# Kernel tuning notes

Hardware: AMD Instinct MI355X
Metric: run time of the kernel (lower is better)

The kernel has to match this reference:

```python
import jax, jax.numpy as jnp
import numpy as np

B, C, D, W, H = 4, 64, 16, 32, 32
K = 2048  # codebook size

def setup_inputs() -> dict:
    key = jax.random.key(0)
    ks = jax.random.split(key, 6)
    return {
        "x": jax.random.normal(ks[0], (B, C, D, W, H), dtype=jnp.float32),
        "codebook": jax.random.normal(ks[1], (K, C), dtype=jnp.float32),
        "w_in": jax.random.normal(ks[2], (C, C), dtype=jnp.float32) * (1.0 / np.sqrt(C)),
        "b_in": jax.random.normal(ks[3], (C,), dtype=jnp.float32) * 0.01,
        "w_out": jax.random.normal(ks[4], (C, C), dtype=jnp.float32) * (1.0 / np.sqrt(C)),
        "b_out": jax.random.normal(ks[5], (C,), dtype=jnp.float32) * 0.01,
    }

def _conv1x1(x, w, b):
    # 1x1x1 Conv3d == channel mixing: x [B,C,D,W,H], w [Cout,Cin]
    return jnp.einsum('oc,bcdwh->bodwh', w, x) + b[None, :, None, None, None]

def _quantize(x, codebook):
    b, c, d, w, h = x.shape
    xf = jnp.moveaxis(x, 1, -1).reshape(b * d * w * h, c)  # [N, C] tokens
    # squared euclidean distances (same argmin as torch.cdist)
    d2 = (jnp.sum(xf * xf, axis=-1, keepdims=True)
          - 2.0 * xf @ codebook.T
          + jnp.sum(codebook * codebook, axis=-1)[None, :])  # [N, K]
    idx = jnp.argmin(d2, axis=-1)  # [N]
    q = codebook[idx]              # [N, C] gather
    sg = jax.lax.stop_gradient
    commitment_loss = jnp.mean((sg(q) - xf) ** 2)
    codebook_loss = jnp.mean((q - sg(xf)) ** 2)
    q_ste = xf + sg(q - xf)  # straight-through
    z = jnp.moveaxis(q_ste.reshape(b, d, w, h, c), -1, 1)  # [B,C,D,W,H]
    return z, codebook_loss, commitment_loss

def reference(x, codebook, w_in, b_in, w_out, b_out):
    pre = _conv1x1(x, w_in, b_in)
    z, cb_loss, cm_loss = _quantize(pre, codebook)
    out = _conv1x1(z, w_out, b_out)
    return out, z, cb_loss, cm_loss
```

## Files before the change

kernel.cpp:

```cpp
#include <hip/hip_runtime.h>

#define CC 64
#define SS 16384
#define NN 65536
#define KK 2048
#define BM 64
#define BMA 128

typedef __attribute__((ext_vector_type(8))) short bf16x8_t;
typedef __attribute__((ext_vector_type(4))) float fx4_t;
#define MFMA16 __builtin_amdgcn_mfma_f32_16x16x32_bf16

__device__ __forceinline__ unsigned short f2bf(float f) {
  unsigned u = __builtin_bit_cast(unsigned, f);
  return (unsigned short)((u + 0x7fff + ((u >> 16) & 1)) >> 16);
}
__device__ __forceinline__ float bf2f(unsigned short h) {
  unsigned u = (unsigned)h << 16;
  return __builtin_bit_cast(float, u);
}
__device__ __forceinline__ void glds16(const void* g, void* l) {
  __builtin_amdgcn_global_load_lds(
      (const __attribute__((address_space(1))) unsigned*)g,
      (__attribute__((address_space(3))) unsigned*)l, 16, 0, 0);
}

__global__ __launch_bounds__(256, 4) void vq_conv_in(
    const float* __restrict__ x, const float* __restrict__ w_in,
    const float* __restrict__ b_in, float* __restrict__ xf) {
  __shared__ float xs[CC][BM];
  __shared__ float wt[CC][CC];
  int t = threadIdx.x;
  int n0 = blockIdx.x * BM;
  int b = n0 >> 14, s0 = n0 & (SS - 1);
  {
    int o = t >> 2, c0 = (t & 3) * 16;
    const float4* wr = (const float4*)(w_in + o * CC + c0);
#pragma unroll
    for (int i = 0; i < 4; ++i) {
      float4 v = wr[i];
      int ci = c0 + 4 * i;
      wt[ci + 0][o] = v.x; wt[ci + 1][o] = v.y;
      wt[ci + 2][o] = v.z; wt[ci + 3][o] = v.w;
    }
  }
#pragma unroll
  for (int i = 0; i < 4; ++i) {
    int e4 = t + 256 * i;
    int ci = e4 >> 4, tok4 = (e4 & 15) * 4;
    *(float4*)&xs[ci][tok4] =
        *(const float4*)(x + (size_t)b * CC * SS + (size_t)ci * SS + s0 + tok4);
  }
  __syncthreads();
  int tx = t & 15, ty = t >> 4;
  double acc[4][4];
#pragma unroll
  for (int j = 0; j < 4; ++j) {
    double bj = (double)b_in[tx * 4 + j];
#pragma unroll
    for (int m = 0; m < 4; ++m) acc[m][j] = bj;
  }
#pragma unroll 8
  for (int ci = 0; ci < CC; ++ci) {
    float4 xq = *(const float4*)&xs[ci][ty * 4];
    float4 wq = *(const float4*)&wt[ci][tx * 4];
    double xm[4] = {xq.x, xq.y, xq.z, xq.w};
    double wm[4] = {wq.x, wq.y, wq.z, wq.w};
#pragma unroll
    for (int m = 0; m < 4; ++m)
#pragma unroll
      for (int j = 0; j < 4; ++j) acc[m][j] = fma(xm[m], wm[j], acc[m][j]);
  }
#pragma unroll
  for (int j = 0; j < 4; ++j) {
    float4 ov = make_float4((float)acc[0][j], (float)acc[1][j],
                            (float)acc[2][j], (float)acc[3][j]);
    *(float4*)(xf + (size_t)b * CC * SS + (size_t)(tx * 4 + j) * SS + s0 +
               ty * 4) = ov;
  }
}

__global__ __launch_bounds__(256) void vq_split(
    const float* __restrict__ cb, unsigned short* __restrict__ cbh,
    unsigned short* __restrict__ cbl, float* __restrict__ ch) {
  int k = blockIdx.x * 256 + threadIdx.x;
  const float4* r = (const float4*)(cb + (size_t)k * CC);
  unsigned* oh = (unsigned*)(cbh + (size_t)k * CC);
  unsigned* ol = (unsigned*)(cbl + (size_t)k * CC);
  float s = 0.f;
#pragma unroll
  for (int i = 0; i < 16; ++i) {
    float4 v = r[i];
    float vv[4] = {v.x, v.y, v.z, v.w};
    unsigned short h[4], l[4];
#pragma unroll
    for (int u = 0; u < 4; ++u) {
      s = fmaf(vv[u], vv[u], s);
      h[u] = f2bf(vv[u]);
      l[u] = f2bf(vv[u] - bf2f(h[u]));
    }
    oh[2 * i + 0] = (unsigned)h[0] | ((unsigned)h[1] << 16);
    oh[2 * i + 1] = (unsigned)h[2] | ((unsigned)h[3] << 16);
    ol[2 * i + 0] = (unsigned)l[0] | ((unsigned)l[1] << 16);
    ol[2 * i + 1] = (unsigned)l[2] | ((unsigned)l[3] << 16);
  }
  ch[k] = -0.5f * s;
}

__global__ __launch_bounds__(256, 4) void vq_mfma_argmin(
    const float* __restrict__ xf, const unsigned char* __restrict__ cbh,
    const unsigned char* __restrict__ cbl, const float* __restrict__ ch,
    int* __restrict__ cidx) {
  __shared__ __align__(16) unsigned char smem[36864];
  int t = threadIdx.x;
  int kh = blockIdx.x & 1;
  int n0 = (blockIdx.x >> 1) * BMA;
  int b = n0 >> 14, s0 = n0 & (SS - 1);
  int lane = t & 63, w = t >> 6;
  glds16((const unsigned char*)ch + kh * 4096 + w * 1024 + lane * 16,
         smem + 32768 + w * 1024);
  {
    int tok = t & 127;
    int half = t >> 7;
    const float* xb = xf + (size_t)b * CC * SS + s0 + tok;
#pragma unroll
    for (int i = 0; i < 4; ++i) {
      int c0 = half * 32 + i * 8;
      bf16x8_t h8, l8;
#pragma unroll
      for (int j = 0; j < 8; ++j) {
        float v = xb[(size_t)(c0 + j) * SS];
        unsigned short hs = f2bf(v);
        h8[j] = (short)hs;
        l8[j] = (short)f2bf(v - bf2f(hs));
      }
      int ad = tok * 128 + ((half * 64 + i * 16) ^ ((tok & 7) << 4));
      *(bf16x8_t*)(smem + ad) = h8;
      *(bf16x8_t*)(smem + 16384 + ad) = l8;
    }
  }
  __syncthreads();
  int col = lane & 15, quad = lane >> 4;
  bf16x8_t ah[2][2], al[2][2];
#pragma unroll
  for (int rt = 0; rt < 2; ++rt)
#pragma unroll
    for (int kk = 0; kk < 2; ++kk) {
      int tok = w * 32 + rt * 16 + col;
      int ad = tok * 128 + ((kk * 64 + quad * 16) ^ ((tok & 7) << 4));
      ah[rt][kk] = *(const bf16x8_t*)(smem + ad);
      al[rt][kk] = *(const bf16x8_t*)(smem + 16384 + ad);
    }
  __syncthreads();
  float best[2][4];
  int bi[2][4];
#pragma unroll
  for (int rt = 0; rt < 2; ++rt)
#pragma unroll
    for (int r = 0; r < 4; ++r) {
      best[rt][r] = -3.402823466e+38f;
      bi[rt][r] = 0;
    }
  int srcoff = (lane * 16) ^ (((lane >> 3) & 7) << 4);
  const unsigned char* ghh = cbh + (size_t)kh * 131072;
  const unsigned char* glh = cbl + (size_t)kh * 131072;
  glds16(ghh + w * 2048 + srcoff, smem + w * 2048);
  glds16(ghh + w * 2048 + 1024 + srcoff, smem + w * 2048 + 1024);
  glds16(glh + w * 2048 + srcoff, smem + 8192 + w * 2048);
  glds16(glh + w * 2048 + 1024 + srcoff, smem + 8192 + w * 2048 + 1024);
  __syncthreads();
  int swz = (col & 7) << 4;
  int cbo0 = col * 128 + ((quad * 16) ^ swz);
  int cbo1 = col * 128 + ((64 + quad * 16) ^ swz);
  int kcol = kh * 1024 + col;
  const int NT = 16;
  for (int kt = 0; kt < NT; ++kt) {
    unsigned char* bufc = smem + (kt & 1) * 16384;
    unsigned char* bufn = smem + ((kt + 1) & 1) * 16384;
    if (kt + 1 < NT) {
      size_t gof = (size_t)(kt + 1) * 8192 + w * 2048 + srcoff;
      glds16(ghh + gof, bufn + w * 2048);
      glds16(ghh + gof + 1024, bufn + w * 2048 + 1024);
      glds16(glh + gof, bufn + 8192 + w * 2048);
      glds16(glh + gof + 1024, bufn + 8192 + w * 2048 + 1024);
    }
    const unsigned char* cnb = smem + 32768 + kt * 256 + col * 4;
    int kbt = kcol + kt * 64;
#pragma unroll
    for (int sub = 0; sub < 4; ++sub) {
      bf16x8_t bh0 = *(const bf16x8_t*)(bufc + cbo0 + 2048 * sub);
      bf16x8_t bh1 = *(const bf16x8_t*)(bufc + cbo1 + 2048 * sub);
      bf16x8_t bl0 = *(const bf16x8_t*)(bufc + 8192 + cbo0 + 2048 * sub);
      bf16x8_t bl1 = *(const bf16x8_t*)(bufc + 8192 + cbo1 + 2048 * sub);
      float cn = *(const float*)(cnb + 64 * sub);
      int kbase = kbt + sub * 16;
#pragma unroll
      for (int rt = 0; rt < 2; ++rt) {
        fx4_t acc = {cn, cn, cn, cn};
        acc = MFMA16(al[rt][0], bh0, acc, 0, 0, 0);
        acc = MFMA16(al[rt][1], bh1, acc, 0, 0, 0);
        acc = MFMA16(ah[rt][0], bl0, acc, 0, 0, 0);
        acc = MFMA16(ah[rt][1], bl1, acc, 0, 0, 0);
        acc = MFMA16(ah[rt][0], bh0, acc, 0, 0, 0);
        acc = MFMA16(ah[rt][1], bh1, acc, 0, 0, 0);
#pragma unroll
        for (int r = 0; r < 4; ++r) {
          float v = acc[r];
          bool g = v > best[rt][r];
          best[rt][r] = g ? v : best[rt][r];
          bi[rt][r] = g ? kbase : bi[rt][r];
        }
      }
    }
    __syncthreads();
  }
  float secd[2][4];
  int si[2][4];
#pragma unroll
  for (int rt = 0; rt < 2; ++rt)
#pragma unroll
    for (int r = 0; r < 4; ++r) {
      secd[rt][r] = -3.402823466e+38f;
      si[rt][r] = 0x7fffffff;
    }
#pragma unroll
  for (int step = 1; step <= 8; step <<= 1) {
#pragma unroll
    for (int rt = 0; rt < 2; ++rt)
#pragma unroll
      for (int r = 0; r < 4; ++r) {
        float ob = __shfl_xor(best[rt][r], step, 64);
        int oi = __shfl_xor(bi[rt][r], step, 64);
        float os = __shfl_xor(secd[rt][r], step, 64);
        int oj = __shfl_xor(si[rt][r], step, 64);
        bool oW = (ob > best[rt][r]) || (ob == best[rt][r] && oi < bi[rt][r]);
        float nb = oW ? ob : best[rt][r];
        int ni = oW ? oi : bi[rt][r];
        float lb = oW ? best[rt][r] : ob;
        int li = oW ? bi[rt][r] : oi;
        float ws = oW ? os : secd[rt][r];
        int wi = oW ? oj : si[rt][r];
        bool sW = (ws > lb) || (ws == lb && wi < li);
        best[rt][r] = nb; bi[rt][r] = ni;
        secd[rt][r] = sW ? ws : lb; si[rt][r] = sW ? wi : li;
      }
  }
  if (col == 0) {
#pragma unroll
    for (int rt = 0; rt < 2; ++rt)
#pragma unroll
      for (int r = 0; r < 4; ++r) {
        int token = n0 + w * 32 + rt * 16 + quad * 4 + r;
        cidx[(size_t)(2 * kh + 0) * NN + token] = bi[rt][r];
        cidx[(size_t)(2 * kh + 1) * NN + token] = si[rt][r];
      }
  }
}

__global__ __launch_bounds__(256, 3) void vq_finish(
    const float* __restrict__ cb, const float* __restrict__ w_out,
    const float* __restrict__ b_out, const int* __restrict__ cidx,
    float* __restrict__ dout, float* __restrict__ loss_acc) {
  __shared__ float qs[CC][BM];
  __shared__ float xs[CC][BM];
  __shared__ float wt[CC][CC];
  __shared__ int ids[BM];
  int t = threadIdx.x;
  int n0 = blockIdx.x * BM;
  int b = n0 >> 14, s0 = n0 & (SS - 1);
  float* zreg = dout + (size_t)NN * CC;
  {
    int o = t >> 2, c0 = (t & 3) * 16;
    const float4* wr = (const float4*)(w_out + o * CC + c0);
#pragma unroll
    for (int i = 0; i < 4; ++i) {
      float4 v = wr[i];
      int ci = c0 + 4 * i;
      wt[ci + 0][o] = v.x; wt[ci + 1][o] = v.y;
      wt[ci + 2][o] = v.z; wt[ci + 3][o] = v.w;
    }
  }
#pragma unroll
  for (int i = 0; i < 4; ++i) {
    int e4 = t + 256 * i;
    int ci = e4 >> 4, tok4 = (e4 & 15) * 4;
    *(float4*)&xs[ci][tok4] = *(const float4*)(zreg + (size_t)b * CC * SS +
                                               (size_t)ci * SS + s0 + tok4);
  }
  __syncthreads();
  {
    int tok = t >> 2, cand = t & 3;
    int kj = cidx[(size_t)cand * NN + n0 + tok];
    const float* cp = cb + (size_t)kj * CC;
    double dj = 0.0;
#pragma unroll 8
    for (int c = 0; c < CC; ++c) {
      double df = (double)xs[c][tok] - (double)cp[c];
      dj = fma(df, df, dj);
    }
#pragma unroll
    for (int step = 1; step <= 2; step <<= 1) {
      double od = __shfl_xor(dj, step, 64);
      int ok = __shfl_xor(kj, step, 64);
      if (od < dj || (od == dj && ok < kj)) { dj = od; kj = ok; }
    }
    if (cand == 0) ids[tok] = kj;
  }
  __syncthreads();
  {
    int tok = t >> 2, c0 = (t & 3) * 16;
    const float4* qr = (const float4*)(cb + (size_t)ids[tok] * CC + c0);
#pragma unroll
    for (int i = 0; i < 4; ++i) {
      float4 v = qr[i];
      int ch = c0 + 4 * i;
      qs[ch + 0][tok] = v.x; qs[ch + 1][tok] = v.y;
      qs[ch + 2][tok] = v.z; qs[ch + 3][tok] = v.w;
    }
  }
  __syncthreads();
  float lsum = 0.f;
#pragma unroll
  for (int i = 0; i < 4; ++i) {
    int e4 = t + 256 * i;
    int ci = e4 >> 4, tok4 = (e4 & 15) * 4;
    float4 qv = *(const float4*)&qs[ci][tok4];
    float4 xv = *(const float4*)&xs[ci][tok4];
    float dx = qv.x - xv.x, dy = qv.y - xv.y;
    float dz = qv.z - xv.z, dw = qv.w - xv.w;
    lsum = fmaf(dx, dx, lsum); lsum = fmaf(dy, dy, lsum);
    lsum = fmaf(dz, dz, lsum); lsum = fmaf(dw, dw, lsum);
    *(float4*)(zreg + (size_t)b * CC * SS + (size_t)ci * SS + s0 + tok4) = qv;
  }
  int tx = t & 15, ty = t >> 4;
  float acc[4][4];
#pragma unroll
  for (int j = 0; j < 4; ++j) {
    float bj = b_out[tx * 4 + j];
#pragma unroll
    for (int m = 0; m < 4; ++m) acc[m][j] = bj;
  }
#pragma unroll 8
  for (int ci = 0; ci < CC; ++ci) {
    float4 xq = *(const float4*)&qs[ci][ty * 4];
    float4 wq = *(const float4*)&wt[ci][tx * 4];
    float xm[4] = {xq.x, xq.y, xq.z, xq.w};
    float wm[4] = {wq.x, wq.y, wq.z, wq.w};
#pragma unroll
    for (int m = 0; m < 4; ++m)
#pragma unroll
      for (int j = 0; j < 4; ++j) acc[m][j] = fmaf(xm[m], wm[j], acc[m][j]);
  }
#pragma unroll
  for (int j = 0; j < 4; ++j) {
    float4 ov = make_float4(acc[0][j], acc[1][j], acc[2][j], acc[3][j]);
    *(float4*)(dout + (size_t)b * CC * SS + (size_t)(tx * 4 + j) * SS + s0 +
               ty * 4) = ov;
  }
#pragma unroll
  for (int off = 32; off > 0; off >>= 1) lsum += __shfl_down(lsum, off, 64);
  __shared__ float wsum[4];
  if ((t & 63) == 0) wsum[t >> 6] = lsum;
  __syncthreads();
  if (t == 0) atomicAdd(loss_acc, wsum[0] + wsum[1] + wsum[2] + wsum[3]);
}

__global__ void vq_finalize(const float* __restrict__ loss_acc,
                            float* __restrict__ dout) {
  float l = loss_acc[0] * (1.0f / (float)((size_t)NN * CC));
  dout[(size_t)2 * NN * CC + 0] = l;
  dout[(size_t)2 * NN * CC + 1] = l;
}

extern "C" void kernel_launch(void* const* d_in, const int* in_sizes, int n_in,
                              void* d_out, int out_size, void* d_ws,
                              size_t ws_size, hipStream_t stream) {
  const float* x = (const float*)d_in[0];
  const float* cb = (const float*)d_in[1];
  const float* w_in = (const float*)d_in[2];
  const float* b_in = (const float*)d_in[3];
  const float* w_out = (const float*)d_in[4];
  const float* b_out = (const float*)d_in[5];
  float* out = (float*)d_out;
  float* zreg = out + (size_t)NN * CC;

  float* loss_acc = (float*)d_ws;
  float* ch = (float*)((char*)d_ws + 1024);
  unsigned short* cbh = (unsigned short*)((char*)d_ws + 16384);
  unsigned short* cbl = (unsigned short*)((char*)d_ws + 16384 + 262144);
  int* cidx = (int*)((char*)d_ws + 16384 + 2 * 262144);

  hipMemsetAsync(d_ws, 0, 4, stream);

  vq_conv_in<<<NN / BM, 256, 0, stream>>>(x, w_in, b_in, zreg);
  vq_split<<<KK / 256, 256, 0, stream>>>(cb, cbh, cbl, ch);
  vq_mfma_argmin<<<(NN / BMA) * 2, 256, 0, stream>>>(
      zreg, (const unsigned char*)cbh, (const unsigned char*)cbl, ch, cidx);
  vq_finish<<<NN / BM, 256, 0, stream>>>(cb, w_out, b_out, cidx, out,
                                         loss_acc);
  vq_finalize<<<1, 1, 0, stream>>>(loss_acc, out);
}
```

Measured before the change: 112.6 us.

## Triple-buffer codebook tiles with vmcnt waits and raise MFMA wave priority

```diff
diff --git a/kernel.cpp b/kernel.cpp
--- a/kernel.cpp
+++ b/kernel.cpp
@@ -111,14 +111,14 @@
     const float* __restrict__ xf, const unsigned char* __restrict__ cbh,
     const unsigned char* __restrict__ cbl, const float* __restrict__ ch,
     int* __restrict__ cidx) {
-  __shared__ __align__(16) unsigned char smem[36864];
+  __shared__ __align__(16) unsigned char smem[53248];
   int t = threadIdx.x;
   int kh = blockIdx.x & 1;
   int n0 = (blockIdx.x >> 1) * BMA;
   int b = n0 >> 14, s0 = n0 & (SS - 1);
   int lane = t & 63, w = t >> 6;
   glds16((const unsigned char*)ch + kh * 4096 + w * 1024 + lane * 16,
-         smem + 32768 + w * 1024);
+         smem + 49152 + w * 1024);
   {
     int tok = t & 127;
     int half = t >> 7;
@@ -164,27 +164,37 @@
   int srcoff = (lane * 16) ^ (((lane >> 3) & 7) << 4);
   const unsigned char* ghh = cbh + (size_t)kh * 131072;
   const unsigned char* glh = cbl + (size_t)kh * 131072;
-  glds16(ghh + w * 2048 + srcoff, smem + w * 2048);
-  glds16(ghh + w * 2048 + 1024 + srcoff, smem + w * 2048 + 1024);
-  glds16(glh + w * 2048 + srcoff, smem + 8192 + w * 2048);
-  glds16(glh + w * 2048 + 1024 + srcoff, smem + 8192 + w * 2048 + 1024);
-  __syncthreads();
+#pragma unroll
+  for (int p = 0; p < 2; ++p) {
+    size_t g = (size_t)p * 8192 + w * 2048 + srcoff;
+    unsigned boff = p * 16384;
+    glds16(ghh + g, smem + boff + w * 2048);
+    glds16(ghh + g + 1024, smem + boff + w * 2048 + 1024);
+    glds16(glh + g, smem + boff + 8192 + w * 2048);
+    glds16(glh + g + 1024, smem + boff + 8192 + w * 2048 + 1024);
+  }
   int swz = (col & 7) << 4;
   int cbo0 = col * 128 + ((quad * 16) ^ swz);
   int cbo1 = col * 128 + ((64 + quad * 16) ^ swz);
   int kcol = kh * 1024 + col;
   const int NT = 16;
+  int cur = 0;
   for (int kt = 0; kt < NT; ++kt) {
-    unsigned char* bufc = smem + (kt & 1) * 16384;
-    unsigned char* bufn = smem + ((kt + 1) & 1) * 16384;
-    if (kt + 1 < NT) {
-      size_t gof = (size_t)(kt + 1) * 8192 + w * 2048 + srcoff;
-      glds16(ghh + gof, bufn + w * 2048);
-      glds16(ghh + gof + 1024, bufn + w * 2048 + 1024);
-      glds16(glh + gof, bufn + 8192 + w * 2048);
-      glds16(glh + gof + 1024, bufn + 8192 + w * 2048 + 1024);
-    }
-    const unsigned char* cnb = smem + 32768 + kt * 256 + col * 4;
+    if (kt + 1 < NT)
+      asm volatile("s_waitcnt vmcnt(4)\n\ts_barrier" ::: "memory");
+    else
+      asm volatile("s_waitcnt vmcnt(0)\n\ts_barrier" ::: "memory");
+    if (kt + 2 < NT) {
+      int nb = cur + 2; if (nb >= 3) nb -= 3;
+      size_t g = (size_t)(kt + 2) * 8192 + w * 2048 + srcoff;
+      unsigned boff = nb * 16384;
+      glds16(ghh + g, smem + boff + w * 2048);
+      glds16(ghh + g + 1024, smem + boff + w * 2048 + 1024);
+      glds16(glh + g, smem + boff + 8192 + w * 2048);
+      glds16(glh + g + 1024, smem + boff + 8192 + w * 2048 + 1024);
+    }
+    unsigned char* bufc = smem + cur * 16384;
+    const unsigned char* cnb = smem + 49152 + kt * 256 + col * 4;
     int kbt = kcol + kt * 64;
 #pragma unroll
     for (int sub = 0; sub < 4; ++sub) {
@@ -197,12 +207,14 @@
 #pragma unroll
       for (int rt = 0; rt < 2; ++rt) {
         fx4_t acc = {cn, cn, cn, cn};
+        __builtin_amdgcn_s_setprio(1);
         acc = MFMA16(al[rt][0], bh0, acc, 0, 0, 0);
         acc = MFMA16(al[rt][1], bh1, acc, 0, 0, 0);
         acc = MFMA16(ah[rt][0], bl0, acc, 0, 0, 0);
         acc = MFMA16(ah[rt][1], bl1, acc, 0, 0, 0);
         acc = MFMA16(ah[rt][0], bh0, acc, 0, 0, 0);
         acc = MFMA16(ah[rt][1], bh1, acc, 0, 0, 0);
+        __builtin_amdgcn_s_setprio(0);
 #pragma unroll
         for (int r = 0; r < 4; ++r) {
           float v = acc[r];
@@ -212,7 +224,7 @@
         }
       }
     }
-    __syncthreads();
+    cur += 1; if (cur == 3) cur = 0;
   }
   float secd[2][4];
   int si[2][4];
```

After: 120.3 us. +6.8%, slower.

## Enlarge argmin token tile to 256 and split codebook into quarters

Applied to the files above, without the earlier changes.

```diff
diff --git a/kernel.cpp b/kernel.cpp
--- a/kernel.cpp
+++ b/kernel.cpp
@@ -5,7 +5,6 @@
 #define NN 65536
 #define KK 2048
 #define BM 64
-#define BMA 128
 
 typedef __attribute__((ext_vector_type(8))) short bf16x8_t;
 typedef __attribute__((ext_vector_type(4))) float fx4_t;
@@ -111,59 +110,66 @@
     const float* __restrict__ xf, const unsigned char* __restrict__ cbh,
     const unsigned char* __restrict__ cbl, const float* __restrict__ ch,
     int* __restrict__ cidx) {
-  __shared__ __align__(16) unsigned char smem[36864];
+  __shared__ __align__(16) unsigned char smem[34816];
   int t = threadIdx.x;
-  int kh = blockIdx.x & 1;
-  int n0 = (blockIdx.x >> 1) * BMA;
+  int q = blockIdx.x & 3;
+  int n0 = (blockIdx.x >> 2) * 256;
   int b = n0 >> 14, s0 = n0 & (SS - 1);
   int lane = t & 63, w = t >> 6;
-  glds16((const unsigned char*)ch + kh * 4096 + w * 1024 + lane * 16,
-         smem + 32768 + w * 1024);
-  {
-    int tok = t & 127;
-    int half = t >> 7;
-    const float* xb = xf + (size_t)b * CC * SS + s0 + tok;
-#pragma unroll
-    for (int i = 0; i < 4; ++i) {
-      int c0 = half * 32 + i * 8;
-      bf16x8_t h8, l8;
-#pragma unroll
-      for (int j = 0; j < 8; ++j) {
-        float v = xb[(size_t)(c0 + j) * SS];
-        unsigned short hs = f2bf(v);
-        h8[j] = (short)hs;
-        l8[j] = (short)f2bf(v - bf2f(hs));
+  int col = lane & 15, quad = lane >> 4;
+  if (w < 2)
+    glds16((const unsigned char*)ch + q * 2048 + w * 1024 + lane * 16,
+           smem + 32768 + w * 1024);
+  bf16x8_t ah[4][2], al[4][2];
+#pragma unroll
+  for (int rnd = 0; rnd < 2; ++rnd) {
+    {
+      int tokL = t & 127;
+      int half = t >> 7;
+      const float* xb = xf + (size_t)b * CC * SS + s0 + rnd * 128 + tokL;
+#pragma unroll
+      for (int i = 0; i < 4; ++i) {
+        int c0 = half * 32 + i * 8;
+        bf16x8_t h8, l8;
+#pragma unroll
+        for (int j = 0; j < 8; ++j) {
+          float v = xb[(size_t)(c0 + j) * SS];
+          unsigned short hs = f2bf(v);
+          h8[j] = (short)hs;
+          l8[j] = (short)f2bf(v - bf2f(hs));
+        }
+        int ad = tokL * 128 + ((half * 64 + i * 16) ^ ((tokL & 7) << 4));
+        *(bf16x8_t*)(smem + ad) = h8;
+        *(bf16x8_t*)(smem + 16384 + ad) = l8;
       }
-      int ad = tok * 128 + ((half * 64 + i * 16) ^ ((tok & 7) << 4));
-      *(bf16x8_t*)(smem + ad) = h8;
-      *(bf16x8_t*)(smem + 16384 + ad) = l8;
-    }
-  }
-  __syncthreads();
-  int col = lane & 15, quad = lane >> 4;
-  bf16x8_t ah[2][2], al[2][2];
-#pragma unroll
-  for (int rt = 0; rt < 2; ++rt)
-#pragma unroll
-    for (int kk = 0; kk < 2; ++kk) {
-      int tok = w * 32 + rt * 16 + col;
-      int ad = tok * 128 + ((kk * 64 + quad * 16) ^ ((tok & 7) << 4));
-      ah[rt][kk] = *(const bf16x8_t*)(smem + ad);
-      al[rt][kk] = *(const bf16x8_t*)(smem + 16384 + ad);
-    }
-  __syncthreads();
-  float best[2][4];
-  int bi[2][4];
-#pragma unroll
-  for (int rt = 0; rt < 2; ++rt)
+    }
+    __syncthreads();
+    if ((w >> 1) == rnd) {
+      int base = (w & 1) * 64;
+#pragma unroll
+      for (int rt = 0; rt < 4; ++rt)
+#pragma unroll
+        for (int kk = 0; kk < 2; ++kk) {
+          int tokL = base + rt * 16 + col;
+          int ad = tokL * 128 + ((kk * 64 + quad * 16) ^ ((tokL & 7) << 4));
+          ah[rt][kk] = *(const bf16x8_t*)(smem + ad);
+          al[rt][kk] = *(const bf16x8_t*)(smem + 16384 + ad);
+        }
+    }
+    __syncthreads();
+  }
+  float best[4][4];
+  int bi[4][4];
+#pragma unroll
+  for (int rt = 0; rt < 4; ++rt)
 #pragma unroll
     for (int r = 0; r < 4; ++r) {
       best[rt][r] = -3.402823466e+38f;
       bi[rt][r] = 0;
     }
   int srcoff = (lane * 16) ^ (((lane >> 3) & 7) << 4);
-  const unsigned char* ghh = cbh + (size_t)kh * 131072;
-  const unsigned char* glh = cbl + (size_t)kh * 131072;
+  const unsigned char* ghh = cbh + (size_t)q * 65536;
+  const unsigned char* glh = cbl + (size_t)q * 65536;
   glds16(ghh + w * 2048 + srcoff, smem + w * 2048);
   glds16(ghh + w * 2048 + 1024 + srcoff, smem + w * 2048 + 1024);
   glds16(glh + w * 2048 + srcoff, smem + 8192 + w * 2048);
@@ -172,8 +178,8 @@
   int swz = (col & 7) << 4;
   int cbo0 = col * 128 + ((quad * 16) ^ swz);
   int cbo1 = col * 128 + ((64 + quad * 16) ^ swz);
-  int kcol = kh * 1024 + col;
-  const int NT = 16;
+  int kcol = q * 512 + col;
+  const int NT = 8;
   for (int kt = 0; kt < NT; ++kt) {
     unsigned char* bufc = smem + (kt & 1) * 16384;
     unsigned char* bufn = smem + ((kt + 1) & 1) * 16384;
@@ -195,7 +201,7 @@
       float cn = *(const float*)(cnb + 64 * sub);
       int kbase = kbt + sub * 16;
 #pragma unroll
-      for (int rt = 0; rt < 2; ++rt) {
+      for (int rt = 0; rt < 4; ++rt) {
         fx4_t acc = {cn, cn, cn, cn};
         acc = MFMA16(al[rt][0], bh0, acc, 0, 0, 0);
         acc = MFMA16(al[rt][1], bh1, acc, 0, 0, 0);
@@ -214,10 +220,10 @@
     }
     __syncthreads();
   }
-  float secd[2][4];
-  int si[2][4];
-#pragma unroll
-  for (int rt = 0; rt < 2; ++rt)
+  float secd[4][4];
+  int si[4][4];
+#pragma unroll
+  for (int rt = 0; rt < 4; ++rt)
 #pragma unroll
     for (int r = 0; r < 4; ++r) {
       secd[rt][r] = -3.402823466e+38f;
@@ -226,7 +232,7 @@
 #pragma unroll
   for (int step = 1; step <= 8; step <<= 1) {
 #pragma unroll
-    for (int rt = 0; rt < 2; ++rt)
+    for (int rt = 0; rt < 4; ++rt)
 #pragma unroll
       for (int r = 0; r < 4; ++r) {
         float ob = __shfl_xor(best[rt][r], step, 64);
@@ -247,12 +253,12 @@
   }
   if (col == 0) {
 #pragma unroll
-    for (int rt = 0; rt < 2; ++rt)
+    for (int rt = 0; rt < 4; ++rt)
 #pragma unroll
       for (int r = 0; r < 4; ++r) {
-        int token = n0 + w * 32 + rt * 16 + quad * 4 + r;
-        cidx[(size_t)(2 * kh + 0) * NN + token] = bi[rt][r];
-        cidx[(size_t)(2 * kh + 1) * NN + token] = si[rt][r];
+        int token = n0 + w * 64 + rt * 16 + quad * 4 + r;
+        cidx[(size_t)(2 * q + 0) * NN + token] = bi[rt][r];
+        cidx[(size_t)(2 * q + 1) * NN + token] = si[rt][r];
       }
   }
 }
@@ -289,22 +295,29 @@
   }
   __syncthreads();
   {
-    int tok = t >> 2, cand = t & 3;
-    int kj = cidx[(size_t)cand * NN + n0 + tok];
-    const float* cp = cb + (size_t)kj * CC;
-    double dj = 0.0;
+    int tok = t >> 2, cp = t & 3;
+    int k0 = cidx[(size_t)cp * NN + n0 + tok];
+    int k1 = cidx[(size_t)(cp + 4) * NN + n0 + tok];
+    const float* c0p = cb + (size_t)k0 * CC;
+    const float* c1p = cb + (size_t)k1 * CC;
+    double d0 = 0.0, d1 = 0.0;
 #pragma unroll 8
     for (int c = 0; c < CC; ++c) {
-      double df = (double)xs[c][tok] - (double)cp[c];
-      dj = fma(df, df, dj);
-    }
+      double xv = (double)xs[c][tok];
+      double f0 = xv - (double)c0p[c];
+      double f1 = xv - (double)c1p[c];
+      d0 = fma(f0, f0, d0);
+      d1 = fma(f1, f1, d1);
+    }
+    double dj = d0; int kj = k0;
+    if (d1 < dj || (d1 == dj && k1 < kj)) { dj = d1; kj = k1; }
 #pragma unroll
     for (int step = 1; step <= 2; step <<= 1) {
       double od = __shfl_xor(dj, step, 64);
       int ok = __shfl_xor(kj, step, 64);
       if (od < dj || (od == dj && ok < kj)) { dj = od; kj = ok; }
     }
-    if (cand == 0) ids[tok] = kj;
+    if (cp == 0) ids[tok] = kj;
   }
   __syncthreads();
   {
@@ -394,7 +407,7 @@
 
   vq_conv_in<<<NN / BM, 256, 0, stream>>>(x, w_in, b_in, zreg);
   vq_split<<<KK / 256, 256, 0, stream>>>(cb, cbh, cbl, ch);
-  vq_mfma_argmin<<<(NN / BMA) * 2, 256, 0, stream>>>(
+  vq_mfma_argmin<<<(NN / 256) * 4, 256, 0, stream>>>(
       zreg, (const unsigned char*)cbh, (const unsigned char*)cbl, ch, cidx);
   vq_finish<<<NN / BM, 256, 0, stream>>>(cb, w_out, b_out, cidx, out,
                                          loss_acc);
```

Result: slower. 221.9 us (+97.0%).
